# Kernel optimization log

Measured on AMD Instinct MI355X. Metric: run time of the kernel, lower is better.

The kernel has to match this reference:

```python
import jax, jax.numpy as jnp
import numpy as np

B, LIN, E, D, N = 32, 2048, 512, 512, 2  # batch, enc len, enc hidden, dec hidden, dec layers


def setup_inputs() -> dict:
    key = jax.random.key(0)
    k1, k2, k3, k4, k5 = jax.random.split(key, 5)
    d_hidden = jax.random.normal(k1, (B, N, D), dtype=jnp.float32)
    encoder_outputs = jax.random.normal(k2, (B, LIN, E), dtype=jnp.float32)
    fan_in = E + N * D
    lim1 = 1.0 / np.sqrt(fan_in)
    W1 = jax.random.uniform(k3, (fan_in, D), minval=-lim1, maxval=lim1, dtype=jnp.float32)
    b1 = jax.random.uniform(k4, (D,), minval=-lim1, maxval=lim1, dtype=jnp.float32)
    lim2 = 1.0 / np.sqrt(D)
    w2 = jax.random.uniform(k5, (D,), minval=-lim2, maxval=lim2, dtype=jnp.float32)
    return {"d_hidden": d_hidden, "encoder_outputs": encoder_outputs,
            "W1": W1, "b1": b1, "w2": w2}


def reference(d_hidden, encoder_outputs, W1, b1, w2):
    # Faithful to: tanh(Linear(cat(repeat(d_hidden), enc))) -> Linear(.,1) -> softmax
    # cat@W1 == d_flat@W1_d + enc@W1_e (broadcast-add avoids materializing the concat).
    nd = d_hidden.shape[1] * d_hidden.shape[2]
    d_flat = d_hidden.reshape(d_hidden.shape[0], nd)        # [B, N*D]
    W1_d, W1_e = W1[:nd], W1[nd:]                            # [N*D,D], [E,D]
    dec_proj = d_flat @ W1_d + b1                            # [B, D]
    enc_proj = jnp.einsum('ble,ed->bld', encoder_outputs, W1_e)  # [B, Lin, D]
    attn_hidden = jnp.tanh(enc_proj + dec_proj[:, None, :])  # [B, Lin, D]
    scores = jnp.einsum('bld,d->bl', attn_hidden, w2)        # [B, Lin]
    return jax.nn.softmax(scores, axis=-1)
```

## Files before the change

### kernel.cpp

```cpp
#include <hip/hip_runtime.h>
#include <hip/hip_bf16.h>

#define L_SZ 2048
#define E_SZ 512
#define D_SZ 512
#define ND   1024
#define WS_DEC_OFF 0
#define WS_BT_OFF  (32*512*4)
#define WS_SC_OFF  (32*512*4 + 512*512*2)

typedef unsigned short ushort_t;
typedef unsigned int   uint_t;
typedef __attribute__((ext_vector_type(8))) short short8;
typedef __attribute__((ext_vector_type(4))) float floatx4;

__device__ __forceinline__ ushort_t f2bf(float f) {
  uint_t u = __builtin_bit_cast(uint_t, f);
  u += 0x7fffu + ((u >> 16) & 1u);
  return (ushort_t)(u >> 16);
}

__device__ __forceinline__ float fast_tanh(float x) {
  float e = __expf(2.0f * x);
  return 1.0f - 2.0f * __builtin_amdgcn_rcpf(e + 1.0f);
}

__device__ __forceinline__ void dma16(const ushort_t* g, ushort_t* l) {
  __builtin_amdgcn_global_load_lds(
      (const __attribute__((address_space(1))) uint_t*)(const void*)g,
      (__attribute__((address_space(3))) uint_t*)(void*)l,
      16, 0, 0);
}

__global__ __launch_bounds__(256) void prep_k(const float* __restrict__ dh,
                                              const float* __restrict__ W1,
                                              const float* __restrict__ b1,
                                              float* __restrict__ dec,
                                              ushort_t* __restrict__ Bt) {
  int blk = blockIdx.x, t = threadIdx.x;
  if (blk < 256) {
    int b = blk >> 3, d = (blk & 7) * 64 + (t & 63);
    int q = t >> 6;
    __shared__ float red[4][64];
    const float* dfb = dh + b * ND;
    float s = 0.f;
    #pragma unroll 8
    for (int k = q * 256; k < q * 256 + 256; k++)
      s = fmaf(dfb[k], W1[k * D_SZ + d], s);
    red[q][t & 63] = s;
    __syncthreads();
    if (q == 0)
      dec[b * D_SZ + d] = red[0][t] + red[1][t] + red[2][t] + red[3][t] + b1[d];
  } else {
    int tid = blk - 256;
    int tk = (tid >> 4) * 32, tn = (tid & 15) * 32;
    __shared__ float tile[32][33];
    int cc = t & 31, r8 = t >> 5;
    #pragma unroll
    for (int p = 0; p < 4; p++) {
      int r = r8 + p * 8;
      tile[r][cc] = W1[(ND + tk + r) * D_SZ + tn + cc];
    }
    __syncthreads();
    #pragma unroll
    for (int p = 0; p < 4; p++) {
      int nn = r8 + p * 8;
      Bt[(tn + nn) * E_SZ + tk + cc] = f2bf(tile[cc][nn]);
    }
  }
}

__global__ __launch_bounds__(512, 4) void main_k(const float* __restrict__ enc,
                                                 const ushort_t* __restrict__ Bt,
                                                 const float* __restrict__ dec,
                                                 const float* __restrict__ w2,
                                                 float* __restrict__ scores) {
  const int b  = blockIdx.y;
  const int l0 = blockIdx.x * 64;
  const int t  = threadIdx.x;
  const int wave = t >> 6, lane = t & 63;
  const int col = lane & 15, quad = lane >> 4;

  __shared__ ushort_t As[64 * 64];
  __shared__ ushort_t Bs[512 * 64];
  __shared__ float s_sc[64];

  if (t < 64) s_sc[t] = 0.f;

  floatx4 acc[4][4];
  #pragma unroll
  for (int mt = 0; mt < 4; mt++)
    #pragma unroll
    for (int nt = 0; nt < 4; nt++)
      acc[mt][nt] = (floatx4){0.f, 0.f, 0.f, 0.f};

  const float* arow = enc + (size_t)(b * L_SZ + l0) * E_SZ;

  const int am = t >> 3, ac = t & 7;
  const float* aptr = arow + am * E_SZ + ac * 8;
  ushort_t* awr = &As[am * 64 + ((ac ^ (am & 7)) << 3)];

  const int bn0 = wave * 64 + (lane >> 3);
  const int bc0 = (lane & 7) ^ ((lane >> 3) & 7);
  const ushort_t* bptr0 = Bt + bn0 * E_SZ + bc0 * 8;

  float4 pa = *(const float4*)aptr;
  float4 pb = *(const float4*)(aptr + 4);

  #pragma unroll 1
  for (int kw = 0; kw < 8; kw++) {
    __syncthreads();
    union { short8 v; __hip_bfloat162 h[4]; } pk;
    pk.h[0] = __float22bfloat162_rn(make_float2(pa.x, pa.y));
    pk.h[1] = __float22bfloat162_rn(make_float2(pa.z, pa.w));
    pk.h[2] = __float22bfloat162_rn(make_float2(pb.x, pb.y));
    pk.h[3] = __float22bfloat162_rn(make_float2(pb.z, pb.w));
    *(short8*)awr = pk.v;
    const ushort_t* bp = bptr0 + kw * 64;
    #pragma unroll
    for (int j = 0; j < 8; j++)
      dma16(bp + j * 8 * E_SZ, &Bs[(wave * 512 + j * 64) * 8]);
    __syncthreads();
    if (kw < 7) {
      const float* ap = aptr + (kw + 1) * 64;
      pa = *(const float4*)ap;
      pb = *(const float4*)(ap + 4);
    }
    #pragma unroll
    for (int ks = 0; ks < 2; ks++) {
      short8 af[4], bfr[4];
      #pragma unroll
      for (int mt = 0; mt < 4; mt++) {
        int m = mt * 16 + col;
        af[mt] = *(const short8*)&As[m * 64 + ((((ks << 2) + quad) ^ (m & 7)) << 3)];
      }
      #pragma unroll
      for (int nt = 0; nt < 4; nt++) {
        int n = wave * 64 + nt * 16 + col;
        bfr[nt] = *(const short8*)&Bs[n * 64 + ((((ks << 2) + quad) ^ (n & 7)) << 3)];
      }
      #pragma unroll
      for (int mt = 0; mt < 4; mt++)
        #pragma unroll
        for (int nt = 0; nt < 4; nt++)
          acc[mt][nt] = __builtin_amdgcn_mfma_f32_16x16x32_bf16(af[mt], bfr[nt], acc[mt][nt], 0, 0, 0);
    }
  }

  const float* decb = dec + b * D_SZ;
  float sums[4][4];
  #pragma unroll
  for (int mt = 0; mt < 4; mt++)
    #pragma unroll
    for (int r = 0; r < 4; r++) sums[mt][r] = 0.f;

  #pragma unroll
  for (int nt = 0; nt < 4; nt++) {
    int n = wave * 64 + nt * 16 + col;
    float dv = decb[n];
    float wv = w2[n];
    #pragma unroll
    for (int mt = 0; mt < 4; mt++)
      #pragma unroll
      for (int r = 0; r < 4; r++)
        sums[mt][r] += fast_tanh(acc[mt][nt][r] + dv) * wv;
  }
  #pragma unroll
  for (int mt = 0; mt < 4; mt++) {
    #pragma unroll
    for (int r = 0; r < 4; r++) {
      float v = sums[mt][r];
      v += __shfl_xor(v, 1, 16);
      v += __shfl_xor(v, 2, 16);
      v += __shfl_xor(v, 4, 16);
      v += __shfl_xor(v, 8, 16);
      if (col == 0) atomicAdd(&s_sc[mt * 16 + quad * 4 + r], v);
    }
  }
  __syncthreads();
  if (t < 64) scores[b * L_SZ + l0 + t] = s_sc[t];
}

__global__ __launch_bounds__(1024) void softmax_k(const float* __restrict__ sc,
                                                  float* __restrict__ out) {
  int b = blockIdx.x, t = threadIdx.x;
  int wave = t >> 6, lane = t & 63;
  __shared__ float redm[16], reds[16];
  const float* row = sc + b * L_SZ;
  float v0 = row[t], v1 = row[t + 1024];
  float mx = fmaxf(v0, v1);
  #pragma unroll
  for (int off = 32; off >= 1; off >>= 1) mx = fmaxf(mx, __shfl_xor(mx, off, 64));
  if (lane == 0) redm[wave] = mx;
  __syncthreads();
  float m = redm[0];
  #pragma unroll
  for (int i = 1; i < 16; i++) m = fmaxf(m, redm[i]);
  v0 = __expf(v0 - m);
  v1 = __expf(v1 - m);
  float s = v0 + v1;
  #pragma unroll
  for (int off = 32; off >= 1; off >>= 1) s += __shfl_xor(s, off, 64);
  if (lane == 0) reds[wave] = s;
  __syncthreads();
  float sum = reds[0];
  #pragma unroll
  for (int i = 1; i < 16; i++) sum += reds[i];
  float inv = 1.0f / sum;
  out[b * L_SZ + t]        = v0 * inv;
  out[b * L_SZ + t + 1024] = v1 * inv;
}

extern "C" void kernel_launch(void* const* d_in, const int* in_sizes, int n_in,
                              void* d_out, int out_size, void* d_ws, size_t ws_size,
                              hipStream_t stream) {
  const float* d_hidden = (const float*)d_in[0];
  const float* enc      = (const float*)d_in[1];
  const float* W1       = (const float*)d_in[2];
  const float* b1       = (const float*)d_in[3];
  const float* w2       = (const float*)d_in[4];
  float* out = (float*)d_out;

  char* ws = (char*)d_ws;
  float*    dec = (float*)(ws + WS_DEC_OFF);
  ushort_t* Bt  = (ushort_t*)(ws + WS_BT_OFF);
  float*    sc  = (float*)(ws + WS_SC_OFF);

  prep_k<<<512, 256, 0, stream>>>(d_hidden, W1, b1, dec, Bt);
  main_k<<<dim3(32, 32), 512, 0, stream>>>(enc, Bt, dec, w2, sc);
  softmax_k<<<32, 1024, 0, stream>>>(sc, out);
}
```

Baseline: 237.1 us.

## Split decoder-hidden dimension across two blocks and sum partial scores in softmax

Main kernel now uses a third grid dimension to split the 512-wide D output into two halves, each block with 256 threads handling 64 rows by 256 columns, halving B-tile LDS. Partial scores are written per half and combined in the softmax kernel. The MFMA inner loop is reordered to load one B fragment at a time to reduce register pressure. This raises block count and occupancy but duplicates loading and bf16 conversion of the encoder tile for each half.

```diff
diff --git a/kernel.cpp b/kernel.cpp
--- a/kernel.cpp
+++ b/kernel.cpp
@@ -7,7 +7,7 @@
 #define ND   1024
 #define WS_DEC_OFF 0
 #define WS_BT_OFF  (32*512*4)
-#define WS_SC_OFF  (32*512*4 + 512*512*2)
+#define WS_SP_OFF  (32*512*4 + 512*512*2)
 
 typedef unsigned short ushort_t;
 typedef unsigned int   uint_t;
@@ -70,22 +70,20 @@
   }
 }
 
-__global__ __launch_bounds__(512, 4) void main_k(const float* __restrict__ enc,
+__global__ __launch_bounds__(256, 4) void main_k(const float* __restrict__ enc,
                                                  const ushort_t* __restrict__ Bt,
                                                  const float* __restrict__ dec,
                                                  const float* __restrict__ w2,
-                                                 float* __restrict__ scores) {
+                                                 float* __restrict__ spart) {
   const int b  = blockIdx.y;
   const int l0 = blockIdx.x * 64;
+  const int nh = blockIdx.z;
   const int t  = threadIdx.x;
   const int wave = t >> 6, lane = t & 63;
   const int col = lane & 15, quad = lane >> 4;
 
   __shared__ ushort_t As[64 * 64];
-  __shared__ ushort_t Bs[512 * 64];
-  __shared__ float s_sc[64];
-
-  if (t < 64) s_sc[t] = 0.f;
+  __shared__ ushort_t Bs[256 * 64];
 
   floatx4 acc[4][4];
   #pragma unroll
@@ -96,39 +94,54 @@
 
   const float* arow = enc + (size_t)(b * L_SZ + l0) * E_SZ;
 
-  const int am = t >> 3, ac = t & 7;
-  const float* aptr = arow + am * E_SZ + ac * 8;
-  ushort_t* awr = &As[am * 64 + ((ac ^ (am & 7)) << 3)];
+  const int am0 = t >> 3, ac = t & 7;
+  const int am1 = am0 + 32;
+  const float* aptr0 = arow + am0 * E_SZ + ac * 8;
+  const float* aptr1 = arow + am1 * E_SZ + ac * 8;
+  ushort_t* awr0 = &As[am0 * 64 + ((ac ^ (am0 & 7)) << 3)];
+  ushort_t* awr1 = &As[am1 * 64 + ((ac ^ (am1 & 7)) << 3)];
 
   const int bn0 = wave * 64 + (lane >> 3);
   const int bc0 = (lane & 7) ^ ((lane >> 3) & 7);
-  const ushort_t* bptr0 = Bt + bn0 * E_SZ + bc0 * 8;
-
-  float4 pa = *(const float4*)aptr;
-  float4 pb = *(const float4*)(aptr + 4);
+  const ushort_t* bptr0 = Bt + (size_t)(nh * 256 + bn0) * E_SZ + bc0 * 8;
+
+  float4 pa0 = *(const float4*)aptr0;
+  float4 pb0 = *(const float4*)(aptr0 + 4);
+  float4 pa1 = *(const float4*)aptr1;
+  float4 pb1 = *(const float4*)(aptr1 + 4);
 
   #pragma unroll 1
   for (int kw = 0; kw < 8; kw++) {
     __syncthreads();
-    union { short8 v; __hip_bfloat162 h[4]; } pk;
-    pk.h[0] = __float22bfloat162_rn(make_float2(pa.x, pa.y));
-    pk.h[1] = __float22bfloat162_rn(make_float2(pa.z, pa.w));
-    pk.h[2] = __float22bfloat162_rn(make_float2(pb.x, pb.y));
-    pk.h[3] = __float22bfloat162_rn(make_float2(pb.z, pb.w));
-    *(short8*)awr = pk.v;
+    {
+      union { short8 v; __hip_bfloat162 h[4]; } pk;
+      pk.h[0] = __float22bfloat162_rn(make_float2(pa0.x, pa0.y));
+      pk.h[1] = __float22bfloat162_rn(make_float2(pa0.z, pa0.w));
+      pk.h[2] = __float22bfloat162_rn(make_float2(pb0.x, pb0.y));
+      pk.h[3] = __float22bfloat162_rn(make_float2(pb0.z, pb0.w));
+      *(short8*)awr0 = pk.v;
+      pk.h[0] = __float22bfloat162_rn(make_float2(pa1.x, pa1.y));
+      pk.h[1] = __float22bfloat162_rn(make_float2(pa1.z, pa1.w));
+      pk.h[2] = __float22bfloat162_rn(make_float2(pb1.x, pb1.y));
+      pk.h[3] = __float22bfloat162_rn(make_float2(pb1.z, pb1.w));
+      *(short8*)awr1 = pk.v;
+    }
     const ushort_t* bp = bptr0 + kw * 64;
     #pragma unroll
     for (int j = 0; j < 8; j++)
       dma16(bp + j * 8 * E_SZ, &Bs[(wave * 512 + j * 64) * 8]);
     __syncthreads();
     if (kw < 7) {
-      const float* ap = aptr + (kw + 1) * 64;
-      pa = *(const float4*)ap;
-      pb = *(const float4*)(ap + 4);
+      const float* ap0 = aptr0 + (kw + 1) * 64;
+      const float* ap1 = aptr1 + (kw + 1) * 64;
+      pa0 = *(const float4*)ap0;
+      pb0 = *(const float4*)(ap0 + 4);
+      pa1 = *(const float4*)ap1;
+      pb1 = *(const float4*)(ap1 + 4);
     }
     #pragma unroll
     for (int ks = 0; ks < 2; ks++) {
-      short8 af[4], bfr[4];
+      short8 af[4];
       #pragma unroll
       for (int mt = 0; mt < 4; mt++) {
         int m = mt * 16 + col;
@@ -136,35 +149,37 @@
       }
       #pragma unroll
       for (int nt = 0; nt < 4; nt++) {
-        int n = wave * 64 + nt * 16 + col;
-        bfr[nt] = *(const short8*)&Bs[n * 64 + ((((ks << 2) + quad) ^ (n & 7)) << 3)];
+        int nl = wave * 64 + nt * 16 + col;
+        short8 bfr = *(const short8*)&Bs[nl * 64 + ((((ks << 2) + quad) ^ (nl & 7)) << 3)];
+        #pragma unroll
+        for (int mt = 0; mt < 4; mt++)
+          acc[mt][nt] = __builtin_amdgcn_mfma_f32_16x16x32_bf16(af[mt], bfr, acc[mt][nt], 0, 0, 0);
       }
-      #pragma unroll
-      for (int mt = 0; mt < 4; mt++)
-        #pragma unroll
-        for (int nt = 0; nt < 4; nt++)
-          acc[mt][nt] = __builtin_amdgcn_mfma_f32_16x16x32_bf16(af[mt], bfr[nt], acc[mt][nt], 0, 0, 0);
-    }
-  }
-
-  const float* decb = dec + b * D_SZ;
+    }
+  }
+
+  const float* decb = dec + b * D_SZ + nh * 256;
+  const float* w2b  = w2 + nh * 256;
   float sums[4][4];
   #pragma unroll
   for (int mt = 0; mt < 4; mt++)
     #pragma unroll
     for (int r = 0; r < 4; r++) sums[mt][r] = 0.f;
-
   #pragma unroll
   for (int nt = 0; nt < 4; nt++) {
-    int n = wave * 64 + nt * 16 + col;
-    float dv = decb[n];
-    float wv = w2[n];
+    int nl = wave * 64 + nt * 16 + col;
+    float dv = decb[nl];
+    float wv = w2b[nl];
     #pragma unroll
     for (int mt = 0; mt < 4; mt++)
       #pragma unroll
       for (int r = 0; r < 4; r++)
         sums[mt][r] += fast_tanh(acc[mt][nt][r] + dv) * wv;
   }
+  __syncthreads();
+  float* scf = (float*)&As[0];
+  if (t < 64) scf[t] = 0.f;
+  __syncthreads();
   #pragma unroll
   for (int mt = 0; mt < 4; mt++) {
     #pragma unroll
@@ -174,20 +189,22 @@
       v += __shfl_xor(v, 2, 16);
       v += __shfl_xor(v, 4, 16);
       v += __shfl_xor(v, 8, 16);
-      if (col == 0) atomicAdd(&s_sc[mt * 16 + quad * 4 + r], v);
-    }
-  }
-  __syncthreads();
-  if (t < 64) scores[b * L_SZ + l0 + t] = s_sc[t];
-}
-
-__global__ __launch_bounds__(1024) void softmax_k(const float* __restrict__ sc,
+      if (col == 0) atomicAdd(&scf[mt * 16 + quad * 4 + r], v);
+    }
+  }
+  __syncthreads();
+  if (t < 64) spart[nh * (32 * L_SZ) + b * L_SZ + l0 + t] = scf[t];
+}
+
+__global__ __launch_bounds__(1024) void softmax_k(const float* __restrict__ sp,
                                                   float* __restrict__ out) {
   int b = blockIdx.x, t = threadIdx.x;
   int wave = t >> 6, lane = t & 63;
   __shared__ float redm[16], reds[16];
-  const float* row = sc + b * L_SZ;
-  float v0 = row[t], v1 = row[t + 1024];
+  const float* r0 = sp + b * L_SZ;
+  const float* r1 = sp + 32 * L_SZ + b * L_SZ;
+  float v0 = r0[t] + r1[t];
+  float v1 = r0[t + 1024] + r1[t + 1024];
   float mx = fmaxf(v0, v1);
   #pragma unroll
   for (int off = 32; off >= 1; off >>= 1) mx = fmaxf(mx, __shfl_xor(mx, off, 64));
@@ -224,9 +241,9 @@
   char* ws = (char*)d_ws;
   float*    dec = (float*)(ws + WS_DEC_OFF);
   ushort_t* Bt  = (ushort_t*)(ws + WS_BT_OFF);
-  float*    sc  = (float*)(ws + WS_SC_OFF);
+  float*    sp  = (float*)(ws + WS_SP_OFF);
 
   prep_k<<<512, 256, 0, stream>>>(d_hidden, W1, b1, dec, Bt);
-  main_k<<<dim3(32, 32), 512, 0, stream>>>(enc, Bt, dec, w2, sc);
-  softmax_k<<<32, 1024, 0, stream>>>(sc, out);
-}
+  main_k<<<dim3(32, 32, 2), 256, 0, stream>>>(enc, Bt, dec, w2, sp);
+  softmax_k<<<32, 1024, 0, stream>>>(sp, out);
+}
```

Result: slower. 247.4 us (+4.3%).

## Keep weight slice resident in registers and split decoder columns across blocks

Applied to the files above, without the earlier changes.

The main kernel now splits the 512 decoder columns into two groups per block (grid z). Each block loads its 256-column bf16 weight slice once into registers and reuses it across four 64-row L tiles, streaming only the encoder activations through double-buffered LDS with register prefetch. This removes the repeated per-block reloading of the full weight matrix. Partial scores from the two column groups are summed inside softmax, and the decoder projection uses split-K atomics after a memset, with b1 added later. The costs are heavy register pressure (occupancy hint lowered to 2), encoder rows being converted twice (once per column group), and an extra memset launch.

```diff
diff --git a/kernel.cpp b/kernel.cpp
--- a/kernel.cpp
+++ b/kernel.cpp
@@ -6,8 +6,8 @@
 #define D_SZ 512
 #define ND   1024
 #define WS_DEC_OFF 0
-#define WS_BT_OFF  (32*512*4)
-#define WS_SC_OFF  (32*512*4 + 512*512*2)
+#define WS_BT_OFF  65536
+#define WS_SP_OFF  (65536 + 524288)
 
 typedef unsigned short ushort_t;
 typedef unsigned int   uint_t;
@@ -34,23 +34,25 @@
 
 __global__ __launch_bounds__(256) void prep_k(const float* __restrict__ dh,
                                               const float* __restrict__ W1,
-                                              const float* __restrict__ b1,
                                               float* __restrict__ dec,
                                               ushort_t* __restrict__ Bt) {
   int blk = blockIdx.x, t = threadIdx.x;
   if (blk < 256) {
-    int b = blk >> 3, d = (blk & 7) * 64 + (t & 63);
-    int q = t >> 6;
-    __shared__ float red[4][64];
-    const float* dfb = dh + b * ND;
-    float s = 0.f;
-    #pragma unroll 8
-    for (int k = q * 256; k < q * 256 + 256; k++)
-      s = fmaf(dfb[k], W1[k * D_SZ + d], s);
-    red[q][t & 63] = s;
-    __syncthreads();
-    if (q == 0)
-      dec[b * D_SZ + d] = red[0][t] + red[1][t] + red[2][t] + red[3][t] + b1[d];
+    int b = blk >> 3, kq = blk & 7;
+    __shared__ float sdf[128];
+    if (t < 128) sdf[t] = dh[b * ND + kq * 128 + t];
+    __syncthreads();
+    const float* wrow = W1 + (size_t)kq * 128 * D_SZ;
+    int d0 = t, d1 = t + 256;
+    float s0 = 0.f, s1 = 0.f;
+    #pragma unroll 4
+    for (int k = 0; k < 128; k++) {
+      float dv = sdf[k];
+      s0 = fmaf(dv, wrow[k * D_SZ + d0], s0);
+      s1 = fmaf(dv, wrow[k * D_SZ + d1], s1);
+    }
+    atomicAdd(&dec[b * D_SZ + d0], s0);
+    atomicAdd(&dec[b * D_SZ + d1], s1);
   } else {
     int tid = blk - 256;
     int tk = (tid >> 4) * 32, tn = (tid & 15) * 32;
@@ -70,134 +72,167 @@
   }
 }
 
-__global__ __launch_bounds__(512, 4) void main_k(const float* __restrict__ enc,
+__global__ __launch_bounds__(512, 2) void main_k(const float* __restrict__ enc,
                                                  const ushort_t* __restrict__ Bt,
                                                  const float* __restrict__ dec,
+                                                 const float* __restrict__ b1,
                                                  const float* __restrict__ w2,
-                                                 float* __restrict__ scores) {
-  const int b  = blockIdx.y;
-  const int l0 = blockIdx.x * 64;
-  const int t  = threadIdx.x;
-  const int wave = t >> 6, lane = t & 63;
-  const int col = lane & 15, quad = lane >> 4;
-
-  __shared__ ushort_t As[64 * 64];
-  __shared__ ushort_t Bs[512 * 64];
+                                                 float* __restrict__ spart) {
+  const int lslot = blockIdx.x;
+  const int b     = blockIdx.y;
+  const int cg    = blockIdx.z;
+  const int t     = threadIdx.x;
+  const int wave  = t >> 6, lane = t & 63;
+  const int col   = lane & 15, quad = lane >> 4;
+
+  __shared__ ushort_t lds[2][64 * 256];
   __shared__ float s_sc[64];
 
-  if (t < 64) s_sc[t] = 0.f;
-
-  floatx4 acc[4][4];
-  #pragma unroll
-  for (int mt = 0; mt < 4; mt++)
-    #pragma unroll
-    for (int nt = 0; nt < 4; nt++)
-      acc[mt][nt] = (floatx4){0.f, 0.f, 0.f, 0.f};
-
-  const float* arow = enc + (size_t)(b * L_SZ + l0) * E_SZ;
-
-  const int am = t >> 3, ac = t & 7;
-  const float* aptr = arow + am * E_SZ + ac * 8;
-  ushort_t* awr = &As[am * 64 + ((ac ^ (am & 7)) << 3)];
-
-  const int bn0 = wave * 64 + (lane >> 3);
-  const int bc0 = (lane & 7) ^ ((lane >> 3) & 7);
-  const ushort_t* bptr0 = Bt + bn0 * E_SZ + bc0 * 8;
-
-  float4 pa = *(const float4*)aptr;
-  float4 pb = *(const float4*)(aptr + 4);
+  const int m = t >> 3, ac = t & 7;
+  const float* arow0 = enc + (size_t)(b * L_SZ + lslot * 256 + m) * E_SZ + ac * 8;
+
+  float4 pa[8];
+  #pragma unroll
+  for (int j = 0; j < 4; j++) {
+    pa[2 * j]     = *(const float4*)(arow0 + j * 64);
+    pa[2 * j + 1] = *(const float4*)(arow0 + j * 64 + 4);
+  }
+
+  short8 bf[2][16];
+  {
+    ushort_t* Bsc = &lds[0][0];
+    const ushort_t* btc = Bt + (size_t)cg * 256 * E_SZ;
+    #pragma unroll
+    for (int R = 0; R < 4; R++) {
+      #pragma unroll
+      for (int j = 0; j < 8; j++) {
+        int n = wave * 32 + j * 4 + (lane >> 4);
+        int c = (lane & 15) ^ (n & 7);
+        dma16(btc + (size_t)n * E_SZ + R * 128 + c * 8,
+              &Bsc[(wave * 512 + j * 64) * 8]);
+      }
+      __syncthreads();
+      #pragma unroll
+      for (int nt = 0; nt < 2; nt++) {
+        int n = wave * 32 + nt * 16 + col;
+        #pragma unroll
+        for (int ksr = 0; ksr < 4; ksr++)
+          bf[nt][R * 4 + ksr] =
+              *(const short8*)&Bsc[n * 128 + (((ksr * 4 + quad) ^ (n & 7)) << 3)];
+      }
+      __syncthreads();
+    }
+  }
+
+  floatx4 acc[4][2];
 
   #pragma unroll 1
-  for (int kw = 0; kw < 8; kw++) {
-    __syncthreads();
-    union { short8 v; __hip_bfloat162 h[4]; } pk;
-    pk.h[0] = __float22bfloat162_rn(make_float2(pa.x, pa.y));
-    pk.h[1] = __float22bfloat162_rn(make_float2(pa.z, pa.w));
-    pk.h[2] = __float22bfloat162_rn(make_float2(pb.x, pb.y));
-    pk.h[3] = __float22bfloat162_rn(make_float2(pb.z, pb.w));
-    *(short8*)awr = pk.v;
-    const ushort_t* bp = bptr0 + kw * 64;
-    #pragma unroll
-    for (int j = 0; j < 8; j++)
-      dma16(bp + j * 8 * E_SZ, &Bs[(wave * 512 + j * 64) * 8]);
-    __syncthreads();
-    if (kw < 7) {
-      const float* ap = aptr + (kw + 1) * 64;
-      pa = *(const float4*)ap;
-      pb = *(const float4*)(ap + 4);
-    }
-    #pragma unroll
-    for (int ks = 0; ks < 2; ks++) {
-      short8 af[4], bfr[4];
-      #pragma unroll
-      for (int mt = 0; mt < 4; mt++) {
-        int m = mt * 16 + col;
-        af[mt] = *(const short8*)&As[m * 64 + ((((ks << 2) + quad) ^ (m & 7)) << 3)];
-      }
-      #pragma unroll
-      for (int nt = 0; nt < 4; nt++) {
-        int n = wave * 64 + nt * 16 + col;
-        bfr[nt] = *(const short8*)&Bs[n * 64 + ((((ks << 2) + quad) ^ (n & 7)) << 3)];
-      }
+  for (int tile = 0; tile < 4; tile++) {
+    #pragma unroll
+    for (int mt = 0; mt < 4; mt++)
+      #pragma unroll
+      for (int nt = 0; nt < 2; nt++)
+        acc[mt][nt] = (floatx4){0.f, 0.f, 0.f, 0.f};
+
+    #pragma unroll
+    for (int win = 0; win < 2; win++) {
+      #pragma unroll
+      for (int j = 0; j < 4; j++) {
+        union { short8 v; __hip_bfloat162 h[4]; } pk;
+        float4 f0 = pa[2 * j], f1 = pa[2 * j + 1];
+        pk.h[0] = __float22bfloat162_rn(make_float2(f0.x, f0.y));
+        pk.h[1] = __float22bfloat162_rn(make_float2(f0.z, f0.w));
+        pk.h[2] = __float22bfloat162_rn(make_float2(f1.x, f1.y));
+        pk.h[3] = __float22bfloat162_rn(make_float2(f1.z, f1.w));
+        *(short8*)&lds[win][m * 256 + ((j * 8 + (ac ^ (m & 7))) << 3)] = pk.v;
+      }
+      __syncthreads();
+      {
+        int lt = (win == 0) ? tile : tile + 1;
+        int lw = win ^ 1;
+        if (lt < 4) {
+          const float* ap = arow0 + (size_t)lt * 64 * E_SZ + lw * 256;
+          #pragma unroll
+          for (int j = 0; j < 4; j++) {
+            pa[2 * j]     = *(const float4*)(ap + j * 64);
+            pa[2 * j + 1] = *(const float4*)(ap + j * 64 + 4);
+          }
+        }
+      }
+      #pragma unroll
+      for (int ks = 0; ks < 8; ks++) {
+        short8 af[4];
+        #pragma unroll
+        for (int mt = 0; mt < 4; mt++) {
+          int mm = mt * 16 + col;
+          af[mt] = *(const short8*)&lds[win][mm * 256 + (((ks * 4 + quad) ^ (mm & 7)) << 3)];
+        }
+        #pragma unroll
+        for (int mt = 0; mt < 4; mt++)
+          #pragma unroll
+          for (int nt = 0; nt < 2; nt++)
+            acc[mt][nt] = __builtin_amdgcn_mfma_f32_16x16x32_bf16(
+                af[mt], bf[nt][win * 8 + ks], acc[mt][nt], 0, 0, 0);
+      }
+      __syncthreads();
+    }
+
+    const int l0 = lslot * 256 + tile * 64;
+    float sums[4][4];
+    #pragma unroll
+    for (int mt = 0; mt < 4; mt++)
+      #pragma unroll
+      for (int r = 0; r < 4; r++) sums[mt][r] = 0.f;
+    #pragma unroll
+    for (int nt = 0; nt < 2; nt++) {
+      int n = cg * 256 + wave * 32 + nt * 16 + col;
+      float dv = dec[b * D_SZ + n] + b1[n];
+      float wv = w2[n];
       #pragma unroll
       for (int mt = 0; mt < 4; mt++)
         #pragma unroll
-        for (int nt = 0; nt < 4; nt++)
-          acc[mt][nt] = __builtin_amdgcn_mfma_f32_16x16x32_bf16(af[mt], bfr[nt], acc[mt][nt], 0, 0, 0);
-    }
-  }
-
-  const float* decb = dec + b * D_SZ;
-  float sums[4][4];
-  #pragma unroll
-  for (int mt = 0; mt < 4; mt++)
-    #pragma unroll
-    for (int r = 0; r < 4; r++) sums[mt][r] = 0.f;
-
-  #pragma unroll
-  for (int nt = 0; nt < 4; nt++) {
-    int n = wave * 64 + nt * 16 + col;
-    float dv = decb[n];
-    float wv = w2[n];
-    #pragma unroll
-    for (int mt = 0; mt < 4; mt++)
-      #pragma unroll
-      for (int r = 0; r < 4; r++)
-        sums[mt][r] += fast_tanh(acc[mt][nt][r] + dv) * wv;
-  }
-  #pragma unroll
-  for (int mt = 0; mt < 4; mt++) {
-    #pragma unroll
-    for (int r = 0; r < 4; r++) {
-      float v = sums[mt][r];
-      v += __shfl_xor(v, 1, 16);
-      v += __shfl_xor(v, 2, 16);
-      v += __shfl_xor(v, 4, 16);
-      v += __shfl_xor(v, 8, 16);
-      if (col == 0) atomicAdd(&s_sc[mt * 16 + quad * 4 + r], v);
-    }
-  }
-  __syncthreads();
-  if (t < 64) scores[b * L_SZ + l0 + t] = s_sc[t];
-}
-
-__global__ __launch_bounds__(1024) void softmax_k(const float* __restrict__ sc,
+        for (int r = 0; r < 4; r++)
+          sums[mt][r] += fast_tanh(acc[mt][nt][r] + dv) * wv;
+    }
+    if (t < 64) s_sc[t] = 0.f;
+    __syncthreads();
+    #pragma unroll
+    for (int mt = 0; mt < 4; mt++) {
+      #pragma unroll
+      for (int r = 0; r < 4; r++) {
+        float v = sums[mt][r];
+        v += __shfl_xor(v, 1, 16);
+        v += __shfl_xor(v, 2, 16);
+        v += __shfl_xor(v, 4, 16);
+        v += __shfl_xor(v, 8, 16);
+        if (col == 0) atomicAdd(&s_sc[mt * 16 + quad * 4 + r], v);
+      }
+    }
+    __syncthreads();
+    if (t < 64) spart[(size_t)cg * 32 * L_SZ + b * L_SZ + l0 + t] = s_sc[t];
+    __syncthreads();
+  }
+}
+
+__global__ __launch_bounds__(1024) void softmax_k(const float* __restrict__ sp,
                                                   float* __restrict__ out) {
   int b = blockIdx.x, t = threadIdx.x;
   int wave = t >> 6, lane = t & 63;
   __shared__ float redm[16], reds[16];
-  const float* row = sc + b * L_SZ;
-  float v0 = row[t], v1 = row[t + 1024];
+  const float* r0 = sp + b * L_SZ;
+  const float* r1 = sp + 32 * L_SZ + b * L_SZ;
+  float v0 = r0[t] + r1[t];
+  float v1 = r0[t + 1024] + r1[t + 1024];
   float mx = fmaxf(v0, v1);
   #pragma unroll
   for (int off = 32; off >= 1; off >>= 1) mx = fmaxf(mx, __shfl_xor(mx, off, 64));
   if (lane == 0) redm[wave] = mx;
   __syncthreads();
-  float m = redm[0];
-  #pragma unroll
-  for (int i = 1; i < 16; i++) m = fmaxf(m, redm[i]);
-  v0 = __expf(v0 - m);
-  v1 = __expf(v1 - m);
+  float mm = redm[0];
+  #pragma unroll
+  for (int i = 1; i < 16; i++) mm = fmaxf(mm, redm[i]);
+  v0 = __expf(v0 - mm);
+  v1 = __expf(v1 - mm);
   float s = v0 + v1;
   #pragma unroll
   for (int off = 32; off >= 1; off >>= 1) s += __shfl_xor(s, off, 64);
@@ -224,9 +259,10 @@
   char* ws = (char*)d_ws;
   float*    dec = (float*)(ws + WS_DEC_OFF);
   ushort_t* Bt  = (ushort_t*)(ws + WS_BT_OFF);
-  float*    sc  = (float*)(ws + WS_SC_OFF);
-
-  prep_k<<<512, 256, 0, stream>>>(d_hidden, W1, b1, dec, Bt);
-  main_k<<<dim3(32, 32), 512, 0, stream>>>(enc, Bt, dec, w2, sc);
-  softmax_k<<<32, 1024, 0, stream>>>(sc, out);
-}
+  float*    sp  = (float*)(ws + WS_SP_OFF);
+
+  hipMemsetAsync(dec, 0, 32 * D_SZ * sizeof(float), stream);
+  prep_k<<<512, 256, 0, stream>>>(d_hidden, W1, dec, Bt);
+  main_k<<<dim3(8, 32, 2), 512, 0, stream>>>(enc, Bt, dec, b1, w2, sp);
+  softmax_k<<<32, 1024, 0, stream>>>(sp, out);
+}
```

Result: slower. 263.3 us (+11.0%).
